# Optimization experiments

Measured on AMD Instinct MI355X. Metric: run time of the kernel, lower is better.

The kernel has to match this reference:

```python
import jax, jax.numpy as jnp
import numpy as np

BATCH, SEQ, DIM = 2, 2048, 1024
HEADS, HEAD_DIM = 16, 64
K_NEI = 64
SCALE = 1.0 / float(np.sqrt(HEAD_DIM))


def _cantor_routes(seq_len: int, k: int, depth: int = 8) -> np.ndarray:
    """Replicates _build_positional_routes: Cantor coords + topk smallest |ci-cj|."""
    pos = np.arange(seq_len, dtype=np.float64)
    x = pos / max(1, seq_len - 1)
    x = np.clip(x, 1e-6, 1.0 - 1e-6)
    val = np.zeros_like(x)
    factor = 0.5
    for _ in range(depth):
        xs = x * 3.0
        digit = np.floor(xs)
        x = xs - digit
        val = val + (digit == 2.0).astype(np.float64) * factor
        factor *= 0.5
    val = np.clip(val, 0.0, 1.0)
    dist = np.abs(val[:, None] - val[None, :])  # [S, S]
    routes = np.argsort(dist, axis=1, kind='stable')[:, :k]  # smallest-k neighbors
    return routes.astype(np.int32)


def setup_inputs() -> dict:
    key = jax.random.key(0)
    kx, kw1, kb1, kw2, kb2 = jax.random.split(key, 5)
    x = jax.random.normal(kx, (BATCH, SEQ, DIM), dtype=jnp.float32)
    qkv_w = jax.random.normal(kw1, (3 * DIM, DIM), dtype=jnp.float32) * 0.02
    qkv_b = jax.random.normal(kb1, (3 * DIM,), dtype=jnp.float32) * 0.02
    out_w = jax.random.normal(kw2, (DIM, DIM), dtype=jnp.float32) * 0.02
    out_b = jax.random.normal(kb2, (DIM,), dtype=jnp.float32) * 0.02
    routes = jnp.asarray(_cantor_routes(SEQ, K_NEI))  # [S, K] int32
    return {"x": x, "routes": routes, "qkv_w": qkv_w, "qkv_b": qkv_b,
            "out_w": out_w, "out_b": out_b}


def reference(x, routes, qkv_w, qkv_b, out_w, out_b):
    B, S, _ = x.shape
    # QKV projection (torch Linear: x @ W.T + b)
    qkv = x @ qkv_w.T + qkv_b                          # [B, S, 3*DIM]
    qkv = qkv.reshape(B, S, 3, HEADS, HEAD_DIM).transpose(2, 0, 3, 1, 4)
    q, k, v = qkv[0], qkv[1], qkv[2]                   # each [B, H, S, D]
    # Gather K/V along precomputed Cantor routes: [B, H, S, K, D]
    k_g = jnp.take(k, routes, axis=2)
    v_g = jnp.take(v, routes, axis=2)
    scores = jnp.einsum('bhqd,bhqkd->bhqk', q, k_g) * SCALE
    attn = jax.nn.softmax(scores, axis=-1)             # [B, H, S, K]
    out = jnp.einsum('bhqk,bhqkd->bhqd', attn, v_g)    # [B, H, S, D]
    out = out.transpose(0, 2, 1, 3).reshape(B, S, DIM)
    return out @ out_w.T + out_b
```

## Files before the change

kernel.cpp:

```cpp
#include <hip/hip_runtime.h>
#include <math.h>

#define BATCH    2
#define SEQ      2048
#define DIM      1024
#define HEADS    16
#define HEAD_DIM 64
#define K_NEI    64
#define QKV_DIM  3072
#define MROWS    (BATCH * SEQ)
#define ATT_SCALE 0.125f

typedef _Float16 half8  __attribute__((ext_vector_type(8)));
typedef _Float16 half4  __attribute__((ext_vector_type(4)));
typedef _Float16 half2t __attribute__((ext_vector_type(2)));
typedef float    floatx4 __attribute__((ext_vector_type(4)));

__device__ inline void async_copy16(const void* g, void* l) {
  __builtin_amdgcn_global_load_lds(
      (const __attribute__((address_space(1))) unsigned int*)g,
      (__attribute__((address_space(3))) unsigned int*)l, 16, 0, 0);
}

__device__ inline float dot2h(half2t a, half2t b, float c) {
#if defined(__has_builtin) && __has_builtin(__builtin_amdgcn_fdot2)
  return __builtin_amdgcn_fdot2(a, b, c, false);
#else
  return c + (float)a[0] * (float)b[0] + (float)a[1] * (float)b[1];
#endif
}

__global__ __launch_bounds__(256)
void cast3(const float* __restrict__ a, int na4,
           const float* __restrict__ b, int nb4,
           const float* __restrict__ c, int nc4,
           _Float16* __restrict__ oa, _Float16* __restrict__ ob,
           _Float16* __restrict__ oc) {
  const int total = na4 + nb4 + nc4;
  for (int i = blockIdx.x * blockDim.x + threadIdx.x; i < total;
       i += gridDim.x * blockDim.x) {
    const float* src; _Float16* dst; int idx;
    if (i < na4)            { src = a; dst = oa; idx = i; }
    else if (i < na4 + nb4) { src = b; dst = ob; idx = i - na4; }
    else                    { src = c; dst = oc; idx = i - na4 - nb4; }
    float4 v = *(const float4*)(src + (size_t)idx * 4);
    half4 o;
    o[0] = (_Float16)v.x; o[1] = (_Float16)v.y;
    o[2] = (_Float16)v.z; o[3] = (_Float16)v.w;
    *(half4*)(dst + (size_t)idx * 4) = o;
  }
}

template<int BM, int BN, bool HALF_OUT>
__global__ __launch_bounds__(256)
void gemm_bt_f16(const _Float16* __restrict__ A, const _Float16* __restrict__ B,
                 const float* __restrict__ bias, void* __restrict__ Cv,
                 int M, int N, int K) {
  constexpr int FI = BM / 32;
  constexpr int FJ = BN / 32;
  constexpr int CA = BM / 64;
  constexpr int CB = BN / 64;
  __shared__ _Float16 As[2 * BM * 32];
  __shared__ _Float16 Bs[2 * BN * 32];

  const int tid  = threadIdx.x;
  const int lane = tid & 63;
  const int w    = tid >> 6;
  const int wr   = w >> 1;
  const int wc   = w & 1;
  const int bm   = blockIdx.y * BM;
  const int bn   = blockIdx.x * BN;

  const int srow = w * 16 + (lane >> 2);
  const int scol = (lane & 3) * 8;
  const _Float16* ga = A + (size_t)(bm + srow) * K + scol;
  const _Float16* gb = B + (size_t)(bn + srow) * K + scol;

  const int frow = lane & 15;
  const int fk   = (lane >> 4) * 8;

  floatx4 acc[FI][FJ] = {};

  for (int k0 = 0; k0 < K; k0 += 64) {
#pragma unroll
    for (int sub = 0; sub < 2; sub++) {
      const int kk = k0 + sub * 32;
#pragma unroll
      for (int i = 0; i < CA; i++)
        async_copy16(ga + (size_t)(i * 64) * K + kk,
                     As + sub * BM * 32 + w * 512 + i * 2048);
#pragma unroll
      for (int i = 0; i < CB; i++)
        async_copy16(gb + (size_t)(i * 64) * K + kk,
                     Bs + sub * BN * 32 + w * 512 + i * 2048);
    }
    __syncthreads();

#pragma unroll
    for (int sub = 0; sub < 2; sub++) {
      half8 af[FI], bf[FJ];
#pragma unroll
      for (int i = 0; i < FI; i++)
        af[i] = *(const half8*)&As[sub * BM * 32 + (wr * (BM / 2) + i * 16 + frow) * 32 + fk];
#pragma unroll
      for (int j = 0; j < FJ; j++)
        bf[j] = *(const half8*)&Bs[sub * BN * 32 + (wc * (BN / 2) + j * 16 + frow) * 32 + fk];
#pragma unroll
      for (int i = 0; i < FI; i++)
#pragma unroll
        for (int j = 0; j < FJ; j++) {
          if (HALF_OUT)
            acc[i][j] = __builtin_amdgcn_mfma_f32_16x16x32_f16(bf[j], af[i], acc[i][j], 0, 0, 0);
          else
            acc[i][j] = __builtin_amdgcn_mfma_f32_16x16x32_f16(af[i], bf[j], acc[i][j], 0, 0, 0);
        }
    }
    __syncthreads();
  }

  if (HALF_OUT) {
    _Float16* C = (_Float16*)Cv;
    const int mloc = lane & 15;
    const int nloc = (lane >> 4) * 4;
#pragma unroll
    for (int j = 0; j < FJ; j++) {
      const int gcol = bn + wc * (BN / 2) + j * 16 + nloc;
      float4 bj = *(const float4*)(bias + gcol);
#pragma unroll
      for (int i = 0; i < FI; i++) {
        const int grow = bm + wr * (BM / 2) + i * 16 + mloc;
        half4 hv;
        hv[0] = (_Float16)(acc[i][j][0] + bj.x);
        hv[1] = (_Float16)(acc[i][j][1] + bj.y);
        hv[2] = (_Float16)(acc[i][j][2] + bj.z);
        hv[3] = (_Float16)(acc[i][j][3] + bj.w);
        *(half4*)(C + (size_t)grow * N + gcol) = hv;
      }
    }
  } else {
    float* C = (float*)Cv;
    const int crow = (lane >> 4) * 4;
    const int ccol = lane & 15;
#pragma unroll
    for (int j = 0; j < FJ; j++) {
      const int gcol = bn + wc * (BN / 2) + j * 16 + ccol;
      const float bj = bias[gcol];
#pragma unroll
      for (int i = 0; i < FI; i++) {
        const int grow = bm + wr * (BM / 2) + i * 16 + crow;
        float* cp = C + (size_t)grow * N + gcol;
#pragma unroll
        for (int r = 0; r < 4; r++)
          cp[(size_t)r * N] = acc[i][j][r] + bj;
      }
    }
  }
}

__global__ __launch_bounds__(256)
void attn_kernel(const _Float16* __restrict__ qkv,
                 const int* __restrict__ routes,
                 _Float16* __restrict__ ao) {
  const int lane = threadIdx.x & 63;
  const int w    = threadIdx.x >> 6;
  const int g    = lane >> 4;
  const int c    = lane & 15;

  const int i    = blockIdx.x;
  const int xcd  = i & 7;
  const int j    = i >> 3;
  const int bh   = j >> 6;
  const int qsub = j & 63;
  const int qblk = xcd * 64 + qsub;
  const int q    = qblk * 4 + w;
  const int h    = bh & 15;
  const int b    = bh >> 4;

  __shared__ float scratch[4][16 * 68];
  float* sw = scratch[w];

  const size_t row_base = (size_t)b * SEQ;
  const int    hoff     = h * HEAD_DIM;

  const int* rbase = routes + q * K_NEI + g;
  int rq[16];
#pragma unroll
  for (int t = 0; t < 16; t++) rq[t] = rbase[4 * t];

  const half4 qv = *(const half4*)(qkv + (row_base + q) * QKV_DIM + hoff + 4 * c);
  const half2t qv01 = { qv[0], qv[1] };
  const half2t qv23 = { qv[2], qv[3] };

  half4 vv[16];

#pragma unroll
  for (int t = 0; t < 16; t++) {
    const _Float16* kp = qkv + (row_base + rq[t]) * QKV_DIM + DIM + hoff + 4 * c;
    half4 kv = *(const half4*)kp;
    vv[t]    = *(const half4*)(kp + DIM);
    half2t k01 = { kv[0], kv[1] };
    half2t k23 = { kv[2], kv[3] };
    float sp = dot2h(k23, qv23, dot2h(k01, qv01, 0.f));
    sw[t * 68 + lane] = sp;
  }

  const int rb = (lane >> 2) * 68 + (lane & 3) * 16;
  float4 p0 = *(const float4*)&sw[rb];
  float4 p1 = *(const float4*)&sw[rb + 4];
  float4 p2 = *(const float4*)&sw[rb + 8];
  float4 p3 = *(const float4*)&sw[rb + 12];
  float sc = ((p0.x + p0.y) + (p0.z + p0.w)) + ((p1.x + p1.y) + (p1.z + p1.w))
           + ((p2.x + p2.y) + (p2.z + p2.w)) + ((p3.x + p3.y) + (p3.z + p3.w));

  float m = sc;
#pragma unroll
  for (int off = 1; off < 64; off <<= 1) m = fmaxf(m, __shfl_xor(m, off));
  float e = __expf((sc - m) * ATT_SCALE);
  float sum = e;
#pragma unroll
  for (int off = 1; off < 64; off <<= 1) sum += __shfl_xor(sum, off);
  const float pn = e / sum;

  sw[lane] = pn;
  float o0 = 0.f, o1 = 0.f, o2 = 0.f, o3 = 0.f;
#pragma unroll
  for (int t = 0; t < 16; t++) {
    const float p = sw[4 * t + g];
    o0 += p * (float)vv[t][0];
    o1 += p * (float)vv[t][1];
    o2 += p * (float)vv[t][2];
    o3 += p * (float)vv[t][3];
  }
  o0 += __shfl_xor(o0, 16); o0 += __shfl_xor(o0, 32);
  o1 += __shfl_xor(o1, 16); o1 += __shfl_xor(o1, 32);
  o2 += __shfl_xor(o2, 16); o2 += __shfl_xor(o2, 32);
  o3 += __shfl_xor(o3, 16); o3 += __shfl_xor(o3, 32);

  if (g == 0) {
    half4 hv;
    hv[0] = (_Float16)o0; hv[1] = (_Float16)o1;
    hv[2] = (_Float16)o2; hv[3] = (_Float16)o3;
    *(half4*)(ao + (row_base + q) * DIM + hoff + 4 * c) = hv;
  }
}

extern "C" void kernel_launch(void* const* d_in, const int* in_sizes, int n_in,
                              void* d_out, int out_size, void* d_ws, size_t ws_size,
                              hipStream_t stream) {
  const float* x      = (const float*)d_in[0];
  const int*   routes = (const int*)  d_in[1];
  const float* qkv_w  = (const float*)d_in[2];
  const float* qkv_b  = (const float*)d_in[3];
  const float* out_w  = (const float*)d_in[4];
  const float* out_b  = (const float*)d_in[5];
  float* out = (float*)d_out;

  _Float16* qkvh = (_Float16*)d_ws;
  _Float16* aoh  = qkvh + (size_t)MROWS * QKV_DIM;
  _Float16* xh   = aoh  + (size_t)MROWS * DIM;
  _Float16* wh   = xh   + (size_t)MROWS * DIM;
  _Float16* owh  = wh   + (size_t)QKV_DIM * DIM;

  cast3<<<1024, 256, 0, stream>>>(x, MROWS * DIM / 4,
                                  qkv_w, QKV_DIM * DIM / 4,
                                  out_w, DIM * DIM / 4,
                                  xh, wh, owh);

  {
    dim3 g(QKV_DIM / 128, MROWS / 128);
    gemm_bt_f16<128, 128, true><<<g, 256, 0, stream>>>(xh, wh, qkv_b, qkvh,
                                                       MROWS, QKV_DIM, DIM);
  }

  attn_kernel<<<(BATCH * HEADS * SEQ) / 4, 256, 0, stream>>>(qkvh, routes, aoh);

  {
    dim3 g(DIM / 128, MROWS / 64);
    gemm_bt_f16<64, 128, false><<<g, 256, 0, stream>>>(aoh, owh, out_b, out,
                                                       MROWS, DIM, DIM);
  }
}
```

Baseline: 208.7 us.

## Remap attention so each block handles all heads of one query row

```diff
diff --git a/kernel.cpp b/kernel.cpp
--- a/kernel.cpp
+++ b/kernel.cpp
@@ -163,85 +163,84 @@
                  _Float16* __restrict__ ao) {
   const int lane = threadIdx.x & 63;
   const int w    = threadIdx.x >> 6;
-  const int g    = lane >> 4;
-  const int c    = lane & 15;
 
   const int i    = blockIdx.x;
   const int xcd  = i & 7;
   const int j    = i >> 3;
-  const int bh   = j >> 6;
-  const int qsub = j & 63;
-  const int qblk = xcd * 64 + qsub;
-  const int q    = qblk * 4 + w;
-  const int h    = bh & 15;
-  const int b    = bh >> 4;
+  const int b    = j >> 8;
+  const int q    = xcd * 256 + (j & 255);
 
   __shared__ float scratch[4][16 * 68];
   float* sw = scratch[w];
 
   const size_t row_base = (size_t)b * SEQ;
-  const int    hoff     = h * HEAD_DIM;
-
-  const int* rbase = routes + q * K_NEI + g;
-  int rq[16];
-#pragma unroll
-  for (int t = 0; t < 16; t++) rq[t] = rbase[4 * t];
-
-  const half4 qv = *(const half4*)(qkv + (row_base + q) * QKV_DIM + hoff + 4 * c);
+  const int    rowoff   = 256 * w + 4 * lane;
+
+  const int rt = routes[q * K_NEI + lane];
+
+  const half4 qv = *(const half4*)(qkv + (row_base + q) * QKV_DIM + rowoff);
   const half2t qv01 = { qv[0], qv[1] };
   const half2t qv23 = { qv[2], qv[3] };
 
-  half4 vv[16];
-
+  float s[4];
+#pragma unroll
+  for (int cc = 0; cc < 4; cc++) {
+#pragma unroll
+    for (int t = 0; t < 16; t++) {
+      const int ri = __builtin_amdgcn_readlane(rt, 16 * cc + t);
+      const half4 kv = *(const half4*)(qkv + (row_base + ri) * QKV_DIM + DIM + rowoff);
+      half2t k01 = { kv[0], kv[1] };
+      half2t k23 = { kv[2], kv[3] };
+      sw[t * 68 + lane] = dot2h(k23, qv23, dot2h(k01, qv01, 0.f));
+    }
+    const int rb = (lane & 15) * 68 + (lane >> 4) * 16;
+    float4 p0 = *(const float4*)&sw[rb];
+    float4 p1 = *(const float4*)&sw[rb + 4];
+    float4 p2 = *(const float4*)&sw[rb + 8];
+    float4 p3 = *(const float4*)&sw[rb + 12];
+    s[cc] = ((p0.x + p0.y) + (p0.z + p0.w)) + ((p1.x + p1.y) + (p1.z + p1.w))
+          + ((p2.x + p2.y) + (p2.z + p2.w)) + ((p3.x + p3.y) + (p3.z + p3.w));
+  }
+
+  float m = fmaxf(fmaxf(s[0], s[1]), fmaxf(s[2], s[3]));
+#pragma unroll
+  for (int off = 1; off < 16; off <<= 1) m = fmaxf(m, __shfl_xor(m, off));
+  float e[4];
+  float sum = 0.f;
+#pragma unroll
+  for (int cc = 0; cc < 4; cc++) {
+    e[cc] = __expf((s[cc] - m) * ATT_SCALE);
+    sum += e[cc];
+  }
+#pragma unroll
+  for (int off = 1; off < 16; off <<= 1) sum += __shfl_xor(sum, off);
+  const float rinv = 1.f / sum;
+
+  const int pbase = (lane >> 4) * 68;
+#pragma unroll
+  for (int cc = 0; cc < 4; cc++)
+    sw[pbase + cc * 16 + (lane & 15)] = e[cc];
+
+  float o0 = 0.f, o1 = 0.f, o2 = 0.f, o3 = 0.f;
 #pragma unroll
   for (int t = 0; t < 16; t++) {
-    const _Float16* kp = qkv + (row_base + rq[t]) * QKV_DIM + DIM + hoff + 4 * c;
-    half4 kv = *(const half4*)kp;
-    vv[t]    = *(const half4*)(kp + DIM);
-    half2t k01 = { kv[0], kv[1] };
-    half2t k23 = { kv[2], kv[3] };
-    float sp = dot2h(k23, qv23, dot2h(k01, qv01, 0.f));
-    sw[t * 68 + lane] = sp;
-  }
-
-  const int rb = (lane >> 2) * 68 + (lane & 3) * 16;
-  float4 p0 = *(const float4*)&sw[rb];
-  float4 p1 = *(const float4*)&sw[rb + 4];
-  float4 p2 = *(const float4*)&sw[rb + 8];
-  float4 p3 = *(const float4*)&sw[rb + 12];
-  float sc = ((p0.x + p0.y) + (p0.z + p0.w)) + ((p1.x + p1.y) + (p1.z + p1.w))
-           + ((p2.x + p2.y) + (p2.z + p2.w)) + ((p3.x + p3.y) + (p3.z + p3.w));
-
-  float m = sc;
-#pragma unroll
-  for (int off = 1; off < 64; off <<= 1) m = fmaxf(m, __shfl_xor(m, off));
-  float e = __expf((sc - m) * ATT_SCALE);
-  float sum = e;
-#pragma unroll
-  for (int off = 1; off < 64; off <<= 1) sum += __shfl_xor(sum, off);
-  const float pn = e / sum;
-
-  sw[lane] = pn;
-  float o0 = 0.f, o1 = 0.f, o2 = 0.f, o3 = 0.f;
-#pragma unroll
-  for (int t = 0; t < 16; t++) {
-    const float p = sw[4 * t + g];
-    o0 += p * (float)vv[t][0];
-    o1 += p * (float)vv[t][1];
-    o2 += p * (float)vv[t][2];
-    o3 += p * (float)vv[t][3];
-  }
-  o0 += __shfl_xor(o0, 16); o0 += __shfl_xor(o0, 32);
-  o1 += __shfl_xor(o1, 16); o1 += __shfl_xor(o1, 32);
-  o2 += __shfl_xor(o2, 16); o2 += __shfl_xor(o2, 32);
-  o3 += __shfl_xor(o3, 16); o3 += __shfl_xor(o3, 32);
-
-  if (g == 0) {
-    half4 hv;
-    hv[0] = (_Float16)o0; hv[1] = (_Float16)o1;
-    hv[2] = (_Float16)o2; hv[3] = (_Float16)o3;
-    *(half4*)(ao + (row_base + q) * DIM + hoff + 4 * c) = hv;
-  }
+    const float4 pv = *(const float4*)&sw[pbase + 4 * t];
+#pragma unroll
+    for (int jj = 0; jj < 4; jj++) {
+      const int ri = __builtin_amdgcn_readlane(rt, 4 * t + jj);
+      const half4 vv = *(const half4*)(qkv + (row_base + ri) * QKV_DIM + 2 * DIM + rowoff);
+      const float p = (jj == 0) ? pv.x : (jj == 1) ? pv.y : (jj == 2) ? pv.z : pv.w;
+      o0 += p * (float)vv[0];
+      o1 += p * (float)vv[1];
+      o2 += p * (float)vv[2];
+      o3 += p * (float)vv[3];
+    }
+  }
+
+  half4 hv;
+  hv[0] = (_Float16)(o0 * rinv); hv[1] = (_Float16)(o1 * rinv);
+  hv[2] = (_Float16)(o2 * rinv); hv[3] = (_Float16)(o3 * rinv);
+  *(half4*)(ao + (row_base + q) * DIM + rowoff) = hv;
 }
 
 extern "C" void kernel_launch(void* const* d_in, const int* in_sizes, int n_in,
@@ -272,7 +271,7 @@
                                                        MROWS, QKV_DIM, DIM);
   }
 
-  attn_kernel<<<(BATCH * HEADS * SEQ) / 4, 256, 0, stream>>>(qkvh, routes, aoh);
+  attn_kernel<<<BATCH * SEQ, 256, 0, stream>>>(qkvh, routes, aoh);
 
   {
     dim3 g(DIM / 128, MROWS / 64);
```

New measurement: 220.5 us. 1.06x slower.
